# Kernel optimization log

Hardware: AMD Instinct MI355X
Metric: run time of the kernel (lower is better)

The kernel has to match this reference:

```python
import jax, jax.numpy as jnp
import numpy as np

HIDDEN = 1024
HEADS = 16
HEAD_DIM = HIDDEN // HEADS


def setup_inputs() -> dict:
    key = jax.random.key(0)
    ks = jax.random.split(key, 9)
    B, S = 4, 2048
    s = 1.0 / np.sqrt(HIDDEN)
    return {
        "inputs": jax.random.normal(ks[0], (B, S, HIDDEN), dtype=jnp.float32),
        "Wq": jax.random.normal(ks[1], (HIDDEN, HIDDEN), dtype=jnp.float32) * s,
        "bq": jnp.zeros((HIDDEN,), dtype=jnp.float32),
        "Wk": jax.random.normal(ks[2], (HIDDEN, HIDDEN), dtype=jnp.float32) * s,
        "bk": jnp.zeros((HIDDEN,), dtype=jnp.float32),
        "Wv": jax.random.normal(ks[3], (HIDDEN, HIDDEN), dtype=jnp.float32) * s,
        "bv": jnp.zeros((HIDDEN,), dtype=jnp.float32),
        "Wp": jax.random.normal(ks[4], (HIDDEN, HIDDEN), dtype=jnp.float32) * s,
        "bp": jnp.zeros((HIDDEN,), dtype=jnp.float32),
        "heads_z": jnp.ones((1, HEADS, 1, 1), dtype=jnp.float32),
        "hidden_z": jnp.ones((HIDDEN,), dtype=jnp.float32),
    }


def _split_heads(x):
    # [B,S,HIDDEN] -> [B,H,S,Dh]
    B, S, _ = x.shape
    return x.reshape(B, S, HEADS, HEAD_DIM).transpose(0, 2, 1, 3)


def reference(inputs, Wq, bq, Wk, bk, Wv, bv, Wp, bp, heads_z, hidden_z):
    q = _split_heads(inputs @ Wq.T + bq)
    k = _split_heads(inputs @ Wk.T + bk)
    v = _split_heads(inputs @ Wv.T + bv)
    scores = jnp.einsum("bhqd,bhkd->bhqk", q, k) / jnp.sqrt(
        jnp.asarray(HEAD_DIM, dtype=q.dtype))
    probs = jax.nn.softmax(scores, axis=-1)
    ctx = jnp.einsum("bhqk,bhkd->bhqd", probs, v)  # [B,H,S,Dh]
    ctx = ctx * heads_z
    B, H, S, D = ctx.shape
    ctx = ctx.transpose(0, 2, 1, 3).reshape(B, S, H * D)
    out = ctx @ Wp.T + bp
    out = out * hidden_z
    return out
```

## Files before the change

kernel.cpp:

```cpp
#include <hip/hip_runtime.h>
#include <hip/hip_bf16.h>

#define HID 1024
#define NH 16
#define DH 64
#define SEQ 2048
#define NB 4
#define MTOT (NB*SEQ)
#define SM_SCALE 0.18033688f

typedef __attribute__((ext_vector_type(4))) float f32x4;
typedef __attribute__((ext_vector_type(16))) float f32x16;
typedef __attribute__((ext_vector_type(8))) __bf16 bf16x8;
typedef __attribute__((ext_vector_type(4))) __bf16 bf16x4;
typedef __attribute__((ext_vector_type(2))) __bf16 bf16x2;
typedef __attribute__((ext_vector_type(2))) int i32x2;

__device__ __forceinline__ f32x4 mfma16(bf16x8 a, bf16x8 b, f32x4 c) {
    return __builtin_amdgcn_mfma_f32_16x16x32_bf16(a, b, c, 0, 0, 0);
}
__device__ __forceinline__ f32x16 mfma32(bf16x8 a, bf16x8 b, f32x16 c) {
    return __builtin_amdgcn_mfma_f32_32x32x16_bf16(a, b, c, 0, 0, 0);
}

__device__ __forceinline__ void gload16(const void* g, void* l) {
    __builtin_amdgcn_global_load_lds(
        (const __attribute__((address_space(1))) unsigned int*)g,
        (__attribute__((address_space(3))) unsigned int*)l, 16, 0, 0);
}

__device__ __forceinline__ float fexp2(float x) {
#if __has_builtin(__builtin_amdgcn_exp2f)
    return __builtin_amdgcn_exp2f(x);
#else
    return exp2f(x);
#endif
}

__device__ __forceinline__ unsigned pkbf2(float lo, float hi) {
    union { bf16x2 v; unsigned u; } c;
    c.v = (bf16x2){ (__bf16)lo, (__bf16)hi };
    return c.u;
}

#define F3(a,b,c) fmaxf(fmaxf((a),(b)),(c))

__device__ __forceinline__ void swap32(unsigned &a, unsigned &b) {
#if __has_builtin(__builtin_amdgcn_permlane32_swap)
    i32x2 r = __builtin_amdgcn_permlane32_swap((int)a, (int)b, false, false);
    a = (unsigned)r.x; b = (unsigned)r.y;
#else
    const bool hi = (threadIdx.x & 32) != 0;
    unsigned ta = __shfl_xor(a, 32), tb = __shfl_xor(b, 32);
    unsigned na = hi ? tb : a;
    unsigned nb = hi ? b : ta;
    a = na; b = nb;
#endif
}

__device__ __forceinline__ float swapmaxf(float x) {
    unsigned a = __float_as_uint(x), b = a;
    swap32(a, b);
    return fmaxf(__uint_as_float(a), __uint_as_float(b));
}

__global__ __launch_bounds__(256)
void cvt5(const float* __restrict__ X,  const float* __restrict__ Wq,
          const float* __restrict__ Wk, const float* __restrict__ Wv,
          const float* __restrict__ Wp,
          __bf16* __restrict__ Xb,  __bf16* __restrict__ Wqb,
          __bf16* __restrict__ Wkb, __bf16* __restrict__ Wvb,
          __bf16* __restrict__ Wpb)
{
    const float* src; __bf16* dst; int n;
    switch (blockIdx.y) {
        case 0:  src = X;  dst = Xb;  n = MTOT * HID; break;
        case 1:  src = Wq; dst = Wqb; n = HID * HID;  break;
        case 2:  src = Wk; dst = Wkb; n = HID * HID;  break;
        case 3:  src = Wv; dst = Wvb; n = HID * HID;  break;
        default: src = Wp; dst = Wpb; n = HID * HID;  break;
    }
    const int stride = gridDim.x * 256 * 4;
    for (int i = (blockIdx.x * 256 + threadIdx.x) * 4; i < n; i += stride) {
        float4 v = *(const float4*)(src + i);
        bf16x4 o = { (__bf16)v.x, (__bf16)v.y, (__bf16)v.z, (__bf16)v.w };
        *(bf16x4*)(dst + i) = o;
    }
}

template<int PROJ>
__global__ __launch_bounds__(512, 1)
void gemm8(const __bf16* __restrict__ A,
           const __bf16* __restrict__ Wq, const __bf16* __restrict__ Wk,
           const __bf16* __restrict__ Wv,
           const float* __restrict__ bq, const float* __restrict__ bk,
           const float* __restrict__ bv, const float* __restrict__ hz,
           __bf16* __restrict__ Qo, __bf16* __restrict__ Ko,
           __bf16* __restrict__ Vo, float* __restrict__ Po)
{
    __shared__ __bf16 As[3][256 * 64];
    __shared__ __bf16 Bs[3][128 * 64];
    const int tid = threadIdx.x, lane = tid & 63, wid = tid >> 6;
    const int m0 = blockIdx.x * 256, n0 = blockIdx.y * 128;
    const int wr = wid >> 1, wc = wid & 1;
    const int mode = PROJ ? 3 : (int)blockIdx.z;

    const __bf16* W    = PROJ ? Wq : (mode == 0 ? Wq : mode == 1 ? Wk : Wv);
    const float*  bias = PROJ ? bq : (mode == 0 ? bq : mode == 1 ? bk : bv);

    const int cA0 = tid, cA1 = tid + 512, cA2 = tid + 1024, cA3 = tid + 1536;
    const int cB0 = tid, cB1 = tid + 512;
    const __bf16* aA0 = A + (size_t)(m0 + (cA0 >> 3)) * HID + ((cA0 & 7) ^ ((cA0 >> 3) & 7)) * 8;
    const __bf16* aA1 = A + (size_t)(m0 + (cA1 >> 3)) * HID + ((cA1 & 7) ^ ((cA1 >> 3) & 7)) * 8;
    const __bf16* aA2 = A + (size_t)(m0 + (cA2 >> 3)) * HID + ((cA2 & 7) ^ ((cA2 >> 3) & 7)) * 8;
    const __bf16* aA3 = A + (size_t)(m0 + (cA3 >> 3)) * HID + ((cA3 & 7) ^ ((cA3 >> 3) & 7)) * 8;
    const __bf16* bB0 = W + (size_t)(n0 + (cB0 >> 3)) * HID + ((cB0 & 7) ^ ((cB0 >> 3) & 7)) * 8;
    const __bf16* bB1 = W + (size_t)(n0 + (cB1 >> 3)) * HID + ((cB1 & 7) ^ ((cB1 >> 3) & 7)) * 8;

#define STAGE_A(sl, j) do { char* d_ = (char*)&As[sl][0]; int kk_ = (j) * 64; \
    gload16(aA0 + kk_, d_ + cA0 * 16); gload16(aA1 + kk_, d_ + cA1 * 16);     \
    gload16(aA2 + kk_, d_ + cA2 * 16); gload16(aA3 + kk_, d_ + cA3 * 16); } while (0)
#define STAGE_B(sl, j) do { char* d_ = (char*)&Bs[sl][0]; int kk_ = (j) * 64; \
    gload16(bB0 + kk_, d_ + cB0 * 16); gload16(bB1 + kk_, d_ + cB1 * 16); } while (0)

    f32x4 acc[4][4];
    #pragma unroll
    for (int i = 0; i < 4; i++)
        #pragma unroll
        for (int j = 0; j < 4; j++) acc[i][j] = (f32x4){0.f, 0.f, 0.f, 0.f};

    const int la = lane & 15, lk = lane >> 4;

    STAGE_A(0, 0); STAGE_B(0, 0);
    STAGE_A(1, 1); STAGE_B(1, 1);
    asm volatile("s_waitcnt vmcnt(6)" ::: "memory");
    __builtin_amdgcn_s_barrier();

    int slc = 0;
    for (int j = 0; j < 16; ++j) {
        const char* Ab = (const char*)&As[slc][0];
        const char* Bb = (const char*)&Bs[slc][0];
        const int js = j + 2;
        const int sls = slc == 0 ? 2 : slc - 1;

        bf16x8 af[4][2], bf0[2][2];
        #pragma unroll
        for (int mi = 0; mi < 4; mi++)
            #pragma unroll
            for (int ks = 0; ks < 2; ks++) {
                int row = wr * 64 + mi * 16 + la;
                af[mi][ks] = *(const bf16x8*)(Ab + row * 128 +
                    ((ks * 64 + lk * 16) ^ ((row & 7) << 4)));
            }
        #pragma unroll
        for (int ni = 0; ni < 2; ni++)
            #pragma unroll
            for (int ks = 0; ks < 2; ks++) {
                int row = wc * 64 + ni * 16 + la;
                bf0[ni][ks] = *(const bf16x8*)(Bb + row * 128 +
                    ((ks * 64 + lk * 16) ^ ((row & 7) << 4)));
            }
        if (js < 16) STAGE_A(sls, js);
        __builtin_amdgcn_s_barrier();
        asm volatile("s_waitcnt lgkmcnt(0)" ::: "memory");
        __builtin_amdgcn_sched_barrier(0);
        __builtin_amdgcn_s_setprio(1);
        #pragma unroll
        for (int mi = 0; mi < 4; mi++)
            #pragma unroll
            for (int ni = 0; ni < 2; ni++) {
                acc[mi][ni] = mfma16(af[mi][0], bf0[ni][0], acc[mi][ni]);
                acc[mi][ni] = mfma16(af[mi][1], bf0[ni][1], acc[mi][ni]);
            }
        __builtin_amdgcn_s_setprio(0);
        __builtin_amdgcn_s_barrier();

        bf16x8 bf1[2][2];
        #pragma unroll
        for (int ni = 0; ni < 2; ni++)
            #pragma unroll
            for (int ks = 0; ks < 2; ks++) {
                int row = wc * 64 + (ni + 2) * 16 + la;
                bf1[ni][ks] = *(const bf16x8*)(Bb + row * 128 +
                    ((ks * 64 + lk * 16) ^ ((row & 7) << 4)));
            }
        if (js < 16) STAGE_B(sls, js);
        __builtin_amdgcn_s_barrier();
        asm volatile("s_waitcnt lgkmcnt(0)" ::: "memory");
        __builtin_amdgcn_sched_barrier(0);
        __builtin_amdgcn_s_setprio(1);
        #pragma unroll
        for (int mi = 0; mi < 4; mi++)
            #pragma unroll
            for (int ni = 0; ni < 2; ni++) {
                acc[mi][ni + 2] = mfma16(af[mi][0], bf1[ni][0], acc[mi][ni + 2]);
                acc[mi][ni + 2] = mfma16(af[mi][1], bf1[ni][1], acc[mi][ni + 2]);
            }
        __builtin_amdgcn_s_setprio(0);

        if (j < 13)       { asm volatile("s_waitcnt vmcnt(6)" ::: "memory"); }
        else if (j == 14) { asm volatile("s_waitcnt vmcnt(0)" ::: "memory"); }
        __builtin_amdgcn_s_barrier();

        slc = slc == 2 ? 0 : slc + 1;
    }
#undef STAGE_A
#undef STAGE_B

    if (PROJ) {
        #pragma unroll
        for (int mi = 0; mi < 4; mi++)
            #pragma unroll
            for (int ni = 0; ni < 4; ni++)
                #pragma unroll
                for (int r = 0; r < 4; r++) {
                    int m = m0 + wr * 64 + mi * 16 + lk * 4 + r;
                    int n = n0 + wc * 64 + ni * 16 + la;
                    Po[(size_t)m * HID + n] = (acc[mi][ni][r] + bias[n]) * hz[n];
                }
    } else if (mode == 2) {
        #pragma unroll
        for (int mi = 0; mi < 4; mi++)
            #pragma unroll
            for (int ni = 0; ni < 4; ni++) {
                int m = m0 + wr * 64 + mi * 16 + lk * 4;
                int n = n0 + wc * 64 + ni * 16 + la;
                int b = m >> 11, s = m & (SEQ - 1);
                int h = n >> 6,  d = n & 63;
                bf16x4 o;
                #pragma unroll
                for (int r = 0; r < 4; r++) o[r] = (__bf16)(acc[mi][ni][r] + bias[n]);
                *(bf16x4*)(Vo + ((size_t)(b * NH + h) * DH + d) * SEQ + s) = o;
            }
    } else {
        const float qs = (mode == 0) ? SM_SCALE : 1.0f;
        __bf16* Og = (mode == 0) ? Qo : Ko;
        #pragma unroll
        for (int mi = 0; mi < 4; mi++)
            #pragma unroll
            for (int ni = 0; ni < 4; ni++)
                #pragma unroll
                for (int r = 0; r < 4; r++) {
                    int m = m0 + wr * 64 + mi * 16 + lk * 4 + r;
                    int n = n0 + wc * 64 + ni * 16 + la;
                    float v = (acc[mi][ni][r] + bias[n]) * qs;
                    int b = m >> 11, s = m & (SEQ - 1);
                    int h = n >> 6,  d = n & 63;
                    Og[((size_t)(b * NH + h) * SEQ + s) * DH + d] = (__bf16)v;
                }
    }
}

#define KVB 128

__global__ __launch_bounds__(512, 4)
void attn(const __bf16* __restrict__ Q, const __bf16* __restrict__ K,
          const __bf16* __restrict__ VT, const float* __restrict__ heads_z,
          __bf16* __restrict__ C)
{
    __shared__ __bf16 Ks[2][64 * 128];
    __shared__ __bf16 Vs[2][64 * 128];
    const int tid = threadIdx.x, lane = tid & 63, wid = tid >> 6;
    const int lh = lane >> 5;
    const int id = blockIdx.x;
    const int bh = (id & 7) | ((id >> 6) << 3);
    const int qb = (id >> 3) & 7;
    const int b = bh >> 4, hd = bh & 15;
    const __bf16* Qg = Q + (size_t)bh * SEQ * DH;
    const __bf16* Kg = K + (size_t)bh * SEQ * DH;
    const __bf16* Vg = VT + (size_t)bh * DH * SEQ;
    const int q = qb * 256 + wid * 32 + (lane & 31);
    const int r0 = lane & 31;
    const int kx = (r0 & 15) << 4;

    bf16x8 ones8;
    #pragma unroll
    for (int j = 0; j < 8; j++) ones8[j] = (__bf16)1.0f;

    bf16x8 qf[4];
    #pragma unroll
    for (int s = 0; s < 4; s++)
        qf[s] = *(const bf16x8*)(Qg + (size_t)q * DH + s * 16 + lh * 8);

    f32x16 ctx0, ctx1;
    #pragma unroll
    for (int r = 0; r < 16; r++) { ctx0[r] = 0.f; ctx1[r] = 0.f; }
    float mrun = -1e30f, lrun = 0.f;

    const int kr = tid >> 4;
    const int ks = (tid & 15) ^ (kr & 15);
    const int kda = (ks & 7) * 8;
    const int kvA = kr + ((ks >> 3) << 6);
    const int kvB = kvA + 32;

#define STAGE(buf, kv0_) do {                                                         \
    char* dk_ = (char*)&Ks[buf][0]; char* dv_ = (char*)&Vs[buf][0];                   \
    gload16(Kg + (size_t)((kv0_) + kvA) * DH + kda, dk_ + tid * 16);                  \
    gload16(Kg + (size_t)((kv0_) + kvB) * DH + kda, dk_ + tid * 16 + 8192);           \
    gload16(Vg + (size_t)kr * SEQ + (kv0_) + ks * 8, dv_ + tid * 16);                 \
    gload16(Vg + (size_t)(kr + 32) * SEQ + (kv0_) + ks * 8, dv_ + tid * 16 + 8192);   \
} while (0)

    STAGE(0, 0);
    __syncthreads();

    int cur = 0;
    for (int kv0 = 0; kv0 < SEQ; kv0 += KVB) {
        if (kv0 + KVB < SEQ) STAGE(cur ^ 1, kv0 + KVB);

        #pragma unroll
        for (int hh = 0; hh < 2; hh++) {
            const char* Kb = (const char*)&Ks[cur][0];
            const char* Vb = (const char*)&Vs[cur][0];

            f32x16 st0, st1;
            #pragma unroll
            for (int r = 0; r < 16; r++) { st0[r] = 0.f; st1[r] = 0.f; }
            __builtin_amdgcn_s_setprio(1);
            #pragma unroll
            for (int s = 0; s < 4; s++) {
                int co = (((hh * 8 + 2 * s + lh) << 4)) ^ kx;
                bf16x8 k0 = *(const bf16x8*)(Kb + r0 * 256 + co);
                bf16x8 k1 = *(const bf16x8*)(Kb + (r0 + 32) * 256 + co);
                st0 = mfma32(k0, qf[s], st0);
                st1 = mfma32(k1, qf[s], st1);
            }
            __builtin_amdgcn_s_setprio(0);

            float l1[11];
            l1[0] = F3(st0[0],  st0[1],  st0[2]);
            l1[1] = F3(st0[3],  st0[4],  st0[5]);
            l1[2] = F3(st0[6],  st0[7],  st0[8]);
            l1[3] = F3(st0[9],  st0[10], st0[11]);
            l1[4] = F3(st0[12], st0[13], st0[14]);
            l1[5] = F3(st0[15], st1[0],  st1[1]);
            l1[6] = F3(st1[2],  st1[3],  st1[4]);
            l1[7] = F3(st1[5],  st1[6],  st1[7]);
            l1[8] = F3(st1[8],  st1[9],  st1[10]);
            l1[9] = F3(st1[11], st1[12], st1[13]);
            l1[10] = fmaxf(st1[14], st1[15]);
            float l2a = F3(l1[0], l1[1], l1[2]);
            float l2b = F3(l1[3], l1[4], l1[5]);
            float l2c = F3(l1[6], l1[7], l1[8]);
            float l2d = fmaxf(l1[9], l1[10]);
            float pml = F3(F3(l2a, l2b, l2c), l2d, mrun);
            if (!__all(pml <= mrun + 8.f)) {
                float pm = swapmaxf(pml);
                float nm = fmaxf(mrun, pm);
                float al = fexp2(mrun - nm);
                lrun *= al; mrun = nm;
                #pragma unroll
                for (int r = 0; r < 16; r++) { ctx0[r] *= al; ctx1[r] *= al; }
            }
            const float mneg = -mrun;
            #pragma unroll
            for (int r = 0; r < 16; r++) {
                st0[r] = fexp2(st0[r] + mneg);
                st1[r] = fexp2(st1[r] + mneg);
            }

            unsigned X0 = pkbf2(st0[0],  st0[1]),  X1 = pkbf2(st0[2],  st0[3]);
            unsigned X2 = pkbf2(st0[4],  st0[5]),  X3 = pkbf2(st0[6],  st0[7]);
            unsigned X4 = pkbf2(st0[8],  st0[9]),  X5 = pkbf2(st0[10], st0[11]);
            unsigned X6 = pkbf2(st0[12], st0[13]), X7 = pkbf2(st0[14], st0[15]);
            unsigned Y0 = pkbf2(st1[0],  st1[1]),  Y1 = pkbf2(st1[2],  st1[3]);
            unsigned Y2 = pkbf2(st1[4],  st1[5]),  Y3 = pkbf2(st1[6],  st1[7]);
            unsigned Y4 = pkbf2(st1[8],  st1[9]),  Y5 = pkbf2(st1[10], st1[11]);
            unsigned Y6 = pkbf2(st1[12], st1[13]), Y7 = pkbf2(st1[14], st1[15]);
            swap32(X0, X2); swap32(X1, X3);
            swap32(X4, X6); swap32(X5, X7);
            swap32(Y0, Y2); swap32(Y1, Y3);
            swap32(Y4, Y6); swap32(Y5, Y7);
            union W4 { unsigned w[4]; bf16x8 v; };
            W4 pf[4];
            pf[0].w[0]=X0; pf[0].w[1]=X1; pf[0].w[2]=X2; pf[0].w[3]=X3;
            pf[1].w[0]=X4; pf[1].w[1]=X5; pf[1].w[2]=X6; pf[1].w[3]=X7;
            pf[2].w[0]=Y0; pf[2].w[1]=Y1; pf[2].w[2]=Y2; pf[2].w[3]=Y3;
            pf[3].w[0]=Y4; pf[3].w[1]=Y5; pf[3].w[2]=Y6; pf[3].w[3]=Y7;

            st0[0] = 0.f;
            #pragma unroll
            for (int s = 0; s < 4; s++) st0 = mfma32(ones8, pf[s].v, st0);

            __builtin_amdgcn_s_setprio(1);
            #pragma unroll
            for (int s = 0; s < 4; s++) {
                int co = (((hh * 8 + 2 * s + lh) << 4)) ^ kx;
                bf16x8 v0 = *(const bf16x8*)(Vb + r0 * 256 + co);
                bf16x8 v1 = *(const bf16x8*)(Vb + (r0 + 32) * 256 + co);
                ctx0 = mfma32(v0, pf[s].v, ctx0);
                ctx1 = mfma32(v1, pf[s].v, ctx1);
            }
            __builtin_amdgcn_s_setprio(0);

            lrun += st0[0];
        }

        __syncthreads();
        cur ^= 1;
    }
#undef STAGE

    const float hzv = heads_z[hd];
    const float rl = hzv / lrun;
    __bf16* Crow = C + (size_t)(b * SEQ + q) * HID + hd * DH;
    #pragma unroll
    for (int g = 0; g < 4; g++) {
        bf16x4 o0, o1;
        #pragma unroll
        for (int j = 0; j < 4; j++) {
            o0[j] = (__bf16)(ctx0[4 * g + j] * rl);
            o1[j] = (__bf16)(ctx1[4 * g + j] * rl);
        }
        int d0 = 8 * g + 4 * lh;
        *(bf16x4*)(Crow + d0) = o0;
        *(bf16x4*)(Crow + 32 + d0) = o1;
    }
}

extern "C" void kernel_launch(void* const* d_in, const int* in_sizes, int n_in,
                              void* d_out, int out_size, void* d_ws, size_t ws_size,
                              hipStream_t stream)
{
    const float* X    = (const float*)d_in[0];
    const float* Wq   = (const float*)d_in[1];
    const float* bq   = (const float*)d_in[2];
    const float* Wk   = (const float*)d_in[3];
    const float* bk   = (const float*)d_in[4];
    const float* Wv   = (const float*)d_in[5];
    const float* bv   = (const float*)d_in[6];
    const float* Wp   = (const float*)d_in[7];
    const float* bp   = (const float*)d_in[8];
    const float* hz   = (const float*)d_in[9];
    const float* hidz = (const float*)d_in[10];

    __bf16* ws  = (__bf16*)d_ws;
    __bf16* Xb  = ws;
    __bf16* Wqb = Xb  + (size_t)MTOT * HID;
    __bf16* Wkb = Wqb + (size_t)HID * HID;
    __bf16* Wvb = Wkb + (size_t)HID * HID;
    __bf16* Wpb = Wvb + (size_t)HID * HID;
    __bf16* Qb  = Wpb + (size_t)HID * HID;
    __bf16* Kb  = Qb  + (size_t)MTOT * HID;
    __bf16* VTb = Kb  + (size_t)MTOT * HID;
    __bf16* Cb  = VTb + (size_t)MTOT * HID;

    cvt5<<<dim3(2048, 5), 256, 0, stream>>>(X, Wq, Wk, Wv, Wp, Xb, Wqb, Wkb, Wvb, Wpb);

    gemm8<0><<<dim3(MTOT / 256, HID / 128, 3), 512, 0, stream>>>(
        Xb, Wqb, Wkb, Wvb, bq, bk, bv, nullptr, Qb, Kb, VTb, nullptr);

    attn<<<dim3(512), 512, 0, stream>>>(Qb, Kb, VTb, hz, Cb);

    gemm8<1><<<dim3(MTOT / 256, HID / 128), 512, 0, stream>>>(
        Cb, Wpb, nullptr, nullptr, bp, nullptr, nullptr, hidz,
        nullptr, nullptr, nullptr, (float*)d_out);
}
```

Before: 193.0 us.

## Shrink attention blocks to 4 waves with 64-key tiles and twice the grid

The attention kernel now launches 1024 blocks of 256 threads, each handling 128 queries, where before it launched 512 blocks of 512 threads handling 256 queries. Each iteration stages 64 keys instead of 128 into a halved shared-memory double buffer, using a new swizzled staging layout, and the inner two-half loop is removed. The aim is more resident blocks per CU, better load balance, and less shared memory per block. In exchange, each block reloads K/V for fewer queries, so global K/V traffic doubles, and there are twice as many barriers per key.

```diff
diff --git a/kernel.cpp b/kernel.cpp
--- a/kernel.cpp
+++ b/kernel.cpp
@@ -251,25 +251,23 @@
     }
 }
 
-#define KVB 128
-
-__global__ __launch_bounds__(512, 4)
+__global__ __launch_bounds__(256, 8)
 void attn(const __bf16* __restrict__ Q, const __bf16* __restrict__ K,
           const __bf16* __restrict__ VT, const float* __restrict__ heads_z,
           __bf16* __restrict__ C)
 {
-    __shared__ __bf16 Ks[2][64 * 128];
-    __shared__ __bf16 Vs[2][64 * 128];
+    __shared__ __bf16 Ks[2][32 * 128];
+    __shared__ __bf16 Vs[2][32 * 128];
     const int tid = threadIdx.x, lane = tid & 63, wid = tid >> 6;
     const int lh = lane >> 5;
     const int id = blockIdx.x;
-    const int bh = (id & 7) | ((id >> 6) << 3);
-    const int qb = (id >> 3) & 7;
+    const int bh = (id & 7) | ((id >> 7) << 3);
+    const int qb = (id >> 3) & 15;
     const int b = bh >> 4, hd = bh & 15;
     const __bf16* Qg = Q + (size_t)bh * SEQ * DH;
     const __bf16* Kg = K + (size_t)bh * SEQ * DH;
     const __bf16* Vg = VT + (size_t)bh * DH * SEQ;
-    const int q = qb * 256 + wid * 32 + (lane & 31);
+    const int q = qb * 128 + wid * 32 + (lane & 31);
     const int r0 = lane & 31;
     const int kx = (r0 & 15) << 4;
 
@@ -287,114 +285,113 @@
     for (int r = 0; r < 16; r++) { ctx0[r] = 0.f; ctx1[r] = 0.f; }
     float mrun = -1e30f, lrun = 0.f;
 
-    const int kr = tid >> 4;
-    const int ks = (tid & 15) ^ (kr & 15);
-    const int kda = (ks & 7) * 8;
-    const int kvA = kr + ((ks >> 3) << 6);
-    const int kvB = kvA + 32;
-
-#define STAGE(buf, kv0_) do {                                                         \
-    char* dk_ = (char*)&Ks[buf][0]; char* dv_ = (char*)&Vs[buf][0];                   \
-    gload16(Kg + (size_t)((kv0_) + kvA) * DH + kda, dk_ + tid * 16);                  \
-    gload16(Kg + (size_t)((kv0_) + kvB) * DH + kda, dk_ + tid * 16 + 8192);           \
-    gload16(Vg + (size_t)kr * SEQ + (kv0_) + ks * 8, dv_ + tid * 16);                 \
-    gload16(Vg + (size_t)(kr + 32) * SEQ + (kv0_) + ks * 8, dv_ + tid * 16 + 8192);   \
+    const int row0 = tid >> 4, row1 = row0 + 16;
+    const int sl   = tid & 15;
+    const int ss0  = sl ^ (row0 & 15), ss1 = sl ^ (row1 & 15);
+    const int kvo0 = row0 + ((ss0 >> 3) << 5), kd0 = (ss0 & 7) * 8;
+    const int kvo1 = row1 + ((ss1 >> 3) << 5), kd1 = (ss1 & 7) * 8;
+    const int vd0  = row0 + ((ss0 >> 3) << 5), vk0 = (ss0 & 7) * 8;
+    const int vd1  = row1 + ((ss1 >> 3) << 5), vk1 = (ss1 & 7) * 8;
+
+#define STAGE(buf, kv0_) do {                                                      \
+    char* dk_ = (char*)&Ks[buf][0]; char* dv_ = (char*)&Vs[buf][0];                \
+    gload16(Kg + (size_t)((kv0_) + kvo0) * DH + kd0, dk_ + tid * 16);              \
+    gload16(Kg + (size_t)((kv0_) + kvo1) * DH + kd1, dk_ + (tid + 256) * 16);      \
+    gload16(Vg + (size_t)vd0 * SEQ + (kv0_) + vk0, dv_ + tid * 16);                \
+    gload16(Vg + (size_t)vd1 * SEQ + (kv0_) + vk1, dv_ + (tid + 256) * 16);        \
 } while (0)
 
     STAGE(0, 0);
     __syncthreads();
 
     int cur = 0;
-    for (int kv0 = 0; kv0 < SEQ; kv0 += KVB) {
-        if (kv0 + KVB < SEQ) STAGE(cur ^ 1, kv0 + KVB);
-
-        #pragma unroll
-        for (int hh = 0; hh < 2; hh++) {
-            const char* Kb = (const char*)&Ks[cur][0];
-            const char* Vb = (const char*)&Vs[cur][0];
-
-            f32x16 st0, st1;
-            #pragma unroll
-            for (int r = 0; r < 16; r++) { st0[r] = 0.f; st1[r] = 0.f; }
-            __builtin_amdgcn_s_setprio(1);
-            #pragma unroll
-            for (int s = 0; s < 4; s++) {
-                int co = (((hh * 8 + 2 * s + lh) << 4)) ^ kx;
-                bf16x8 k0 = *(const bf16x8*)(Kb + r0 * 256 + co);
-                bf16x8 k1 = *(const bf16x8*)(Kb + (r0 + 32) * 256 + co);
-                st0 = mfma32(k0, qf[s], st0);
-                st1 = mfma32(k1, qf[s], st1);
-            }
-            __builtin_amdgcn_s_setprio(0);
-
-            float l1[11];
-            l1[0] = F3(st0[0],  st0[1],  st0[2]);
-            l1[1] = F3(st0[3],  st0[4],  st0[5]);
-            l1[2] = F3(st0[6],  st0[7],  st0[8]);
-            l1[3] = F3(st0[9],  st0[10], st0[11]);
-            l1[4] = F3(st0[12], st0[13], st0[14]);
-            l1[5] = F3(st0[15], st1[0],  st1[1]);
-            l1[6] = F3(st1[2],  st1[3],  st1[4]);
-            l1[7] = F3(st1[5],  st1[6],  st1[7]);
-            l1[8] = F3(st1[8],  st1[9],  st1[10]);
-            l1[9] = F3(st1[11], st1[12], st1[13]);
-            l1[10] = fmaxf(st1[14], st1[15]);
-            float l2a = F3(l1[0], l1[1], l1[2]);
-            float l2b = F3(l1[3], l1[4], l1[5]);
-            float l2c = F3(l1[6], l1[7], l1[8]);
-            float l2d = fmaxf(l1[9], l1[10]);
-            float pml = F3(F3(l2a, l2b, l2c), l2d, mrun);
-            if (!__all(pml <= mrun + 8.f)) {
-                float pm = swapmaxf(pml);
-                float nm = fmaxf(mrun, pm);
-                float al = fexp2(mrun - nm);
-                lrun *= al; mrun = nm;
-                #pragma unroll
-                for (int r = 0; r < 16; r++) { ctx0[r] *= al; ctx1[r] *= al; }
-            }
-            const float mneg = -mrun;
-            #pragma unroll
-            for (int r = 0; r < 16; r++) {
-                st0[r] = fexp2(st0[r] + mneg);
-                st1[r] = fexp2(st1[r] + mneg);
-            }
-
-            unsigned X0 = pkbf2(st0[0],  st0[1]),  X1 = pkbf2(st0[2],  st0[3]);
-            unsigned X2 = pkbf2(st0[4],  st0[5]),  X3 = pkbf2(st0[6],  st0[7]);
-            unsigned X4 = pkbf2(st0[8],  st0[9]),  X5 = pkbf2(st0[10], st0[11]);
-            unsigned X6 = pkbf2(st0[12], st0[13]), X7 = pkbf2(st0[14], st0[15]);
-            unsigned Y0 = pkbf2(st1[0],  st1[1]),  Y1 = pkbf2(st1[2],  st1[3]);
-            unsigned Y2 = pkbf2(st1[4],  st1[5]),  Y3 = pkbf2(st1[6],  st1[7]);
-            unsigned Y4 = pkbf2(st1[8],  st1[9]),  Y5 = pkbf2(st1[10], st1[11]);
-            unsigned Y6 = pkbf2(st1[12], st1[13]), Y7 = pkbf2(st1[14], st1[15]);
-            swap32(X0, X2); swap32(X1, X3);
-            swap32(X4, X6); swap32(X5, X7);
-            swap32(Y0, Y2); swap32(Y1, Y3);
-            swap32(Y4, Y6); swap32(Y5, Y7);
-            union W4 { unsigned w[4]; bf16x8 v; };
-            W4 pf[4];
-            pf[0].w[0]=X0; pf[0].w[1]=X1; pf[0].w[2]=X2; pf[0].w[3]=X3;
-            pf[1].w[0]=X4; pf[1].w[1]=X5; pf[1].w[2]=X6; pf[1].w[3]=X7;
-            pf[2].w[0]=Y0; pf[2].w[1]=Y1; pf[2].w[2]=Y2; pf[2].w[3]=Y3;
-            pf[3].w[0]=Y4; pf[3].w[1]=Y5; pf[3].w[2]=Y6; pf[3].w[3]=Y7;
-
-            st0[0] = 0.f;
-            #pragma unroll
-            for (int s = 0; s < 4; s++) st0 = mfma32(ones8, pf[s].v, st0);
-
-            __builtin_amdgcn_s_setprio(1);
-            #pragma unroll
-            for (int s = 0; s < 4; s++) {
-                int co = (((hh * 8 + 2 * s + lh) << 4)) ^ kx;
-                bf16x8 v0 = *(const bf16x8*)(Vb + r0 * 256 + co);
-                bf16x8 v1 = *(const bf16x8*)(Vb + (r0 + 32) * 256 + co);
-                ctx0 = mfma32(v0, pf[s].v, ctx0);
-                ctx1 = mfma32(v1, pf[s].v, ctx1);
-            }
-            __builtin_amdgcn_s_setprio(0);
-
-            lrun += st0[0];
+    for (int kv0 = 0; kv0 < SEQ; kv0 += 64) {
+        if (kv0 + 64 < SEQ) STAGE(cur ^ 1, kv0 + 64);
+
+        const char* Kb = (const char*)&Ks[cur][0];
+        const char* Vb = (const char*)&Vs[cur][0];
+
+        f32x16 st0, st1;
+        #pragma unroll
+        for (int r = 0; r < 16; r++) { st0[r] = 0.f; st1[r] = 0.f; }
+        __builtin_amdgcn_s_setprio(1);
+        #pragma unroll
+        for (int s = 0; s < 4; s++) {
+            int ds = 2 * s + lh;
+            bf16x8 k0 = *(const bf16x8*)(Kb + r0 * 256 + ((ds << 4) ^ kx));
+            bf16x8 k1 = *(const bf16x8*)(Kb + r0 * 256 + (((8 + ds) << 4) ^ kx));
+            st0 = mfma32(k0, qf[s], st0);
+            st1 = mfma32(k1, qf[s], st1);
         }
+        __builtin_amdgcn_s_setprio(0);
+
+        float l1[11];
+        l1[0] = F3(st0[0],  st0[1],  st0[2]);
+        l1[1] = F3(st0[3],  st0[4],  st0[5]);
+        l1[2] = F3(st0[6],  st0[7],  st0[8]);
+        l1[3] = F3(st0[9],  st0[10], st0[11]);
+        l1[4] = F3(st0[12], st0[13], st0[14]);
+        l1[5] = F3(st0[15], st1[0],  st1[1]);
+        l1[6] = F3(st1[2],  st1[3],  st1[4]);
+        l1[7] = F3(st1[5],  st1[6],  st1[7]);
+        l1[8] = F3(st1[8],  st1[9],  st1[10]);
+        l1[9] = F3(st1[11], st1[12], st1[13]);
+        l1[10] = fmaxf(st1[14], st1[15]);
+        float l2a = F3(l1[0], l1[1], l1[2]);
+        float l2b = F3(l1[3], l1[4], l1[5]);
+        float l2c = F3(l1[6], l1[7], l1[8]);
+        float l2d = fmaxf(l1[9], l1[10]);
+        float pml = F3(F3(l2a, l2b, l2c), l2d, mrun);
+        if (!__all(pml <= mrun + 8.f)) {
+            float pm = swapmaxf(pml);
+            float nm = fmaxf(mrun, pm);
+            float al = fexp2(mrun - nm);
+            lrun *= al; mrun = nm;
+            #pragma unroll
+            for (int r = 0; r < 16; r++) { ctx0[r] *= al; ctx1[r] *= al; }
+        }
+        const float mneg = -mrun;
+        #pragma unroll
+        for (int r = 0; r < 16; r++) {
+            st0[r] = fexp2(st0[r] + mneg);
+            st1[r] = fexp2(st1[r] + mneg);
+        }
+
+        unsigned X0 = pkbf2(st0[0],  st0[1]),  X1 = pkbf2(st0[2],  st0[3]);
+        unsigned X2 = pkbf2(st0[4],  st0[5]),  X3 = pkbf2(st0[6],  st0[7]);
+        unsigned X4 = pkbf2(st0[8],  st0[9]),  X5 = pkbf2(st0[10], st0[11]);
+        unsigned X6 = pkbf2(st0[12], st0[13]), X7 = pkbf2(st0[14], st0[15]);
+        unsigned Y0 = pkbf2(st1[0],  st1[1]),  Y1 = pkbf2(st1[2],  st1[3]);
+        unsigned Y2 = pkbf2(st1[4],  st1[5]),  Y3 = pkbf2(st1[6],  st1[7]);
+        unsigned Y4 = pkbf2(st1[8],  st1[9]),  Y5 = pkbf2(st1[10], st1[11]);
+        unsigned Y6 = pkbf2(st1[12], st1[13]), Y7 = pkbf2(st1[14], st1[15]);
+        swap32(X0, X2); swap32(X1, X3);
+        swap32(X4, X6); swap32(X5, X7);
+        swap32(Y0, Y2); swap32(Y1, Y3);
+        swap32(Y4, Y6); swap32(Y5, Y7);
+        union W4 { unsigned w[4]; bf16x8 v; };
+        W4 pf[4];
+        pf[0].w[0]=X0; pf[0].w[1]=X1; pf[0].w[2]=X2; pf[0].w[3]=X3;
+        pf[1].w[0]=X4; pf[1].w[1]=X5; pf[1].w[2]=X6; pf[1].w[3]=X7;
+        pf[2].w[0]=Y0; pf[2].w[1]=Y1; pf[2].w[2]=Y2; pf[2].w[3]=Y3;
+        pf[3].w[0]=Y4; pf[3].w[1]=Y5; pf[3].w[2]=Y6; pf[3].w[3]=Y7;
+
+        st0[0] = 0.f;
+        #pragma unroll
+        for (int s = 0; s < 4; s++) st0 = mfma32(ones8, pf[s].v, st0);
+
+        __builtin_amdgcn_s_setprio(1);
+        #pragma unroll
+        for (int s = 0; s < 4; s++) {
+            int vs = 2 * s + lh;
+            bf16x8 v0 = *(const bf16x8*)(Vb + r0 * 256 + ((vs << 4) ^ kx));
+            bf16x8 v1 = *(const bf16x8*)(Vb + r0 * 256 + (((8 + vs) << 4) ^ kx));
+            ctx0 = mfma32(v0, pf[s].v, ctx0);
+            ctx1 = mfma32(v1, pf[s].v, ctx1);
+        }
+        __builtin_amdgcn_s_setprio(0);
+
+        lrun += st0[0];
 
         __syncthreads();
         cur ^= 1;
@@ -450,7 +447,7 @@
     gemm8<0><<<dim3(MTOT / 256, HID / 128, 3), 512, 0, stream>>>(
         Xb, Wqb, Wkb, Wvb, bq, bk, bv, nullptr, Qb, Kb, VTb, nullptr);
 
-    attn<<<dim3(512), 512, 0, stream>>>(Qb, Kb, VTb, hz, Cb);
+    attn<<<dim3(1024), 256, 0, stream>>>(Qb, Kb, VTb, hz, Cb);
 
     gemm8<1><<<dim3(MTOT / 256, HID / 128), 512, 0, stream>>>(
         Cb, Wpb, nullptr, nullptr, bp, nullptr, nullptr, hidz,
```

Result: slower. 214.2 us (+10.9%).
